# Kernel tuning notes

Measured on AMD Instinct MI355X. Metric: run time of the kernel, lower is better.

The kernel has to match this reference:

```python
import jax, jax.numpy as jnp
import numpy as np

V, E, H, L, B = 32000, 512, 512, 64, 32
H2 = 2 * H  # decoder hidden size
SOS = 127


def lstm_cell(x, h, c, Wih, Whh, b):
    gates = x @ Wih.T + h @ Whh.T + b
    i, f, g, o = jnp.split(gates, 4, axis=-1)
    i = jax.nn.sigmoid(i); f = jax.nn.sigmoid(f); o = jax.nn.sigmoid(o)
    g = jnp.tanh(g)
    c2 = f * c + i * g
    return o * jnp.tanh(c2), c2


def setup_inputs() -> dict:
    key = jax.random.key(0)
    ks = jax.random.split(key, 20)
    s = 0.02
    inp = {
        "x": jax.random.randint(ks[0], (B, L), 0, V),
        "enc_embed": s * jax.random.normal(ks[1], (V, E), jnp.float32),
        "ef_Wih": s * jax.random.normal(ks[2], (4 * H, E), jnp.float32),
        "ef_Whh": s * jax.random.normal(ks[3], (4 * H, H), jnp.float32),
        "ef_b": jnp.zeros((4 * H,), jnp.float32),
        "eb_Wih": s * jax.random.normal(ks[4], (4 * H, E), jnp.float32),
        "eb_Whh": s * jax.random.normal(ks[5], (4 * H, H), jnp.float32),
        "eb_b": jnp.zeros((4 * H,), jnp.float32),
        "dec_embed": s * jax.random.normal(ks[6], (V, H2), jnp.float32),
        "attn_W": s * jax.random.normal(ks[7], (L, 2 * H2), jnp.float32),
        "attn_b": jnp.zeros((L,), jnp.float32),
        "comb_W": s * jax.random.normal(ks[8], (H2, 2 * H2), jnp.float32),
        "comb_b": jnp.zeros((H2,), jnp.float32),
        "d_Wih": s * jax.random.normal(ks[9], (4 * H2, H2), jnp.float32),
        "d_Whh": s * jax.random.normal(ks[10], (4 * H2, H2), jnp.float32),
        "d_b": jnp.zeros((4 * H2,), jnp.float32),
        "out_W": s * jax.random.normal(ks[11], (V, H2), jnp.float32),
        "out_b": jnp.zeros((V,), jnp.float32),
    }
    return inp


def reference(x, enc_embed, ef_Wih, ef_Whh, ef_b, eb_Wih, eb_Whh, eb_b,
              dec_embed, attn_W, attn_b, comb_W, comb_b,
              d_Wih, d_Whh, d_b, out_W, out_b):
    b, seq = x.shape
    emb = enc_embed[x]  # (B, L, E)

    # Encoder: per-timestep bidirectional LSTM cells (each length-1 call),
    # state carried across the unrolled timestep loop.
    def enc_step(carry, xt):
        hf, cf, hb, cb = carry
        hf, cf = lstm_cell(xt, hf, cf, ef_Wih, ef_Whh, ef_b)
        hb, cb = lstm_cell(xt, hb, cb, eb_Wih, eb_Whh, eb_b)
        return (hf, cf, hb, cb), jnp.concatenate([hf, hb], axis=-1)

    z = jnp.zeros((b, ef_Whh.shape[1]), emb.dtype)
    _, enc_outs = jax.lax.scan(enc_step, (z, z, z, z), emb.transpose(1, 0, 2))
    enc_outs = enc_outs.transpose(1, 0, 2)  # (B, L, 2H)

    # Decoder: Bahdanau-style attention + LSTM cell, greedy argmax feedback.
    h2 = d_Whh.shape[1]

    def dec_step(carry, _):
        h, c, tok = carry
        e = dec_embed[tok]  # (B, 2H)
        aw = jax.nn.softmax(jnp.concatenate([e, h], -1) @ attn_W.T + attn_b, axis=-1)  # (B, L)
        ctx = jnp.einsum('bl,bld->bd', aw, enc_outs)  # (B, 2H)
        comb = jax.nn.relu(jnp.concatenate([e, ctx], -1) @ comb_W.T + comb_b)
        h, c = lstm_cell(comb, h, c, d_Wih, d_Whh, d_b)
        logits = jax.nn.log_softmax(h @ out_W.T + out_b, axis=-1)  # (B, V)
        tok = jnp.argmax(logits, axis=-1)
        return (h, c, tok), logits

    h0 = jnp.zeros((b, h2), emb.dtype)
    tok0 = jnp.full((b,), SOS, dtype=x.dtype)
    _, logits = jax.lax.scan(dec_step, (h0, h0, tok0), None, length=seq)
    return logits.transpose(1, 0, 2)  # (B, T, V)
```

## Files before the change

### kernel.cpp

```cpp
#include <hip/hip_runtime.h>
#include <hip/hip_bf16.h>
#include <string.h>

typedef __bf16 bf16;
typedef __attribute__((ext_vector_type(8))) __bf16 bf16x8;
typedef __attribute__((ext_vector_type(2))) __bf16 bf16x2;
typedef __attribute__((ext_vector_type(4))) float  f32x4;
typedef unsigned long long u64;
typedef unsigned char u8;

#define DEV __device__ __forceinline__

constexpr int V = 32000, E = 512, H = 512, L = 64, NB = 32, H2 = 1024, T = 64, SOS = 127;
constexpr int GE = 4 * H;
constexpr int NBLK = 256;

constexpr size_t OFF_GIN    = 0;
constexpr size_t SZ_GIN     = (size_t)2*T*NB*GE*4;
constexpr size_t OFF_ENCOUT = OFF_GIN + SZ_GIN;
constexpr size_t SZ_ENCOUT  = (size_t)NB*L*H2*2;
constexpr size_t OFF_ENCH   = OFF_ENCOUT + SZ_ENCOUT;
constexpr size_t SZ_ENCH    = (size_t)2*2*NB*H*2;
constexpr size_t OFF_DECH   = OFF_ENCH + SZ_ENCH;
constexpr size_t SZ_DECH    = (size_t)2*NB*H2*2;
constexpr size_t OFF_CAT2   = OFF_DECH + SZ_DECH;
constexpr size_t SZ_CAT2    = (size_t)NB*2*H2*2;
constexpr size_t OFF_COMB   = OFF_CAT2 + SZ_CAT2;
constexpr size_t SZ_COMB    = (size_t)NB*H2*2;
constexpr size_t OFF_HH     = OFF_COMB + SZ_COMB;
constexpr size_t SZ_HH      = (size_t)NB*4*H2*4;
constexpr size_t OFF_PMAX   = OFF_HH + SZ_HH;
constexpr size_t SZ_P       = (size_t)2*NBLK*NB*4;
constexpr size_t OFF_PSUM   = OFF_PMAX + SZ_P;
constexpr size_t OFF_PIDX   = OFF_PSUM + SZ_P;
constexpr size_t OFF_LOGZ   = OFF_PIDX + SZ_P;
constexpr size_t SZ_LOGZ    = (size_t)T*NB*4;
constexpr size_t OFF_WEFIH  = OFF_LOGZ + SZ_LOGZ;
constexpr size_t SZ_WENC    = (size_t)GE*E*2;
constexpr size_t OFF_WEFHH  = OFF_WEFIH + SZ_WENC;
constexpr size_t OFF_WEBIH  = OFF_WEFHH + SZ_WENC;
constexpr size_t OFF_WEBHH  = OFF_WEBIH + SZ_WENC;
constexpr size_t OFF_WCOMB  = OFF_WEBHH + SZ_WENC;
constexpr size_t SZ_WCOMB   = (size_t)H2*2*H2*2;
constexpr size_t OFF_WDIH   = OFF_WCOMB + SZ_WCOMB;
constexpr size_t SZ_WDEC    = (size_t)4*H2*H2*2;
constexpr size_t OFF_WDHH   = OFF_WDIH + SZ_WDEC;
constexpr size_t OFF_WOUT   = OFF_WDHH + SZ_WDEC;
constexpr size_t OFF_WOUT8  = OFF_WOUT;
constexpr size_t SZ_WOUT8   = (size_t)V*1024;
constexpr size_t OFF_WDHH8  = OFF_WOUT8 + SZ_WOUT8;
constexpr size_t SZ_WOUT    = (size_t)V*H2*2;
constexpr size_t OFF_WATTN  = OFF_WOUT + SZ_WOUT;
constexpr size_t SZ_WATTN   = (size_t)L*2*H2*2;
constexpr size_t OFF_EMB2   = OFF_WATTN + SZ_WATTN;
constexpr size_t SZ_EMB2    = (size_t)T*NB*E*2;
constexpr size_t OFF_BAR    = OFF_EMB2 + SZ_EMB2;
constexpr int TAG_PT = 0, TAG_C2 = 8192, TAG_CB = 9216, TAG_H = 11264, TAG_E = 13312;
constexpr int BAR_INTS = 15360;
constexpr size_t OFF_H8 = OFF_BAR + 131072;

constexpr int SM_CATF = 65536;
constexpr int SM_REDM = 73728;
constexpr int SM_REDS = 75776;
constexpr int SM_REDI = 77824;
constexpr int SM_SCR  = 79872;
constexpr int SM_HL   = 114688;
constexpr int SM_BYTES = 147456;

DEV f32x4 mfma16(bf16x8 a, bf16x8 b, f32x4 c) {
  return __builtin_amdgcn_mfma_f32_16x16x32_bf16(a, b, c, 0, 0, 0);
}
DEV f32x4 mfma8(long a, long b, f32x4 c) {
  return __builtin_amdgcn_mfma_f32_16x16x32_fp8_fp8(a, b, c, 0, 0, 0);
}
DEV float sigm(float x) { return 1.f / (1.f + __expf(-x)); }
DEV bf16x8 ld8(const bf16* p) { return *(const bf16x8*)p; }

union U16 { u64 u[2]; bf16x8 v8; f32x4 f4; };
union U4  { unsigned int u; bf16x2 v2; float f; };

DEV bf16x8 ld8_dev(const bf16* p) {
  U16 r;
  r.u[0] = __hip_atomic_load((const u64*)p,       __ATOMIC_RELAXED, __HIP_MEMORY_SCOPE_AGENT);
  r.u[1] = __hip_atomic_load((const u64*)(p + 4), __ATOMIC_RELAXED, __HIP_MEMORY_SCOPE_AGENT);
  return r.v8;
}
DEV void st8_dev(bf16* p, bf16x8 v) {
  U16 r; r.v8 = v;
  __hip_atomic_store((u64*)p,       r.u[0], __ATOMIC_RELAXED, __HIP_MEMORY_SCOPE_AGENT);
  __hip_atomic_store((u64*)(p + 4), r.u[1], __ATOMIC_RELAXED, __HIP_MEMORY_SCOPE_AGENT);
}
DEV void st16f_dev(float* p, f32x4 v) {
  U16 r; r.f4 = v;
  __hip_atomic_store((u64*)p,       r.u[0], __ATOMIC_RELAXED, __HIP_MEMORY_SCOPE_AGENT);
  __hip_atomic_store((u64*)(p + 2), r.u[1], __ATOMIC_RELAXED, __HIP_MEMORY_SCOPE_AGENT);
}
DEV float ldf_dev(const float* p) {
  return __hip_atomic_load(p, __ATOMIC_RELAXED, __HIP_MEMORY_SCOPE_AGENT);
}
DEV void stf_dev(float* p, float v) {
  __hip_atomic_store(p, v, __ATOMIC_RELAXED, __HIP_MEMORY_SCOPE_AGENT);
}
DEV int ldi_dev(const int* p) {
  return __hip_atomic_load(p, __ATOMIC_RELAXED, __HIP_MEMORY_SCOPE_AGENT);
}
DEV void sti_dev(int* p, int v) {
  __hip_atomic_store(p, v, __ATOMIC_RELAXED, __HIP_MEMORY_SCOPE_AGENT);
}
DEV void stb_dev(bf16* p, float x) {
  bf16 h = (bf16)x; unsigned short s; memcpy(&s, &h, 2);
  __hip_atomic_store((unsigned short*)p, s, __ATOMIC_RELAXED, __HIP_MEMORY_SCOPE_AGENT);
}
DEV void st2b_dev(bf16* p, bf16x2 v) {
  U4 r; r.v2 = v;
  __hip_atomic_store((unsigned int*)p, r.u, __ATOMIC_RELAXED, __HIP_MEMORY_SCOPE_AGENT);
}
DEV void stb8_dev(u8* p, u8 v) {
  __hip_atomic_store(p, v, __ATOMIC_RELAXED, __HIP_MEMORY_SCOPE_AGENT);
}
DEV u64 ldu64_dev(const u8* p) {
  return __hip_atomic_load((const u64*)p, __ATOMIC_RELAXED, __HIP_MEMORY_SCOPE_AGENT);
}

DEV void tpub(int* tags, int slot, int ep) {
  __syncthreads();
  if (threadIdx.x == 0)
    sti_dev(tags + slot*32, ep);
}
DEV void twait(int* tags, int n, int ep) {
  if ((int)threadIdx.x < n)
    while (ldi_dev(tags + threadIdx.x*32) < ep)
      __builtin_amdgcn_s_sleep(1);
  asm volatile("" ::: "memory");
  __syncthreads();
}

struct ConvJobs { const float* src[7]; bf16* dst[7]; long n8[7]; };

__global__ __launch_bounds__(256) void k_convert_all(ConvJobs J) {
  long i0 = (long)blockIdx.x * 256 + threadIdx.x;
  long stride = (long)gridDim.x * 256;
  for (int j = 0; j < 7; ++j) {
    const float* __restrict__ src = J.src[j];
    bf16* __restrict__ dst = J.dst[j];
    long n8 = J.n8[j];
    for (long g = i0; g < n8; g += stride) {
      long o = g * 8;
      float4 a = *(const float4*)(src + o);
      float4 b = *(const float4*)(src + o + 4);
      bf16x8 v;
      v[0]=(bf16)a.x; v[1]=(bf16)a.y; v[2]=(bf16)a.z; v[3]=(bf16)a.w;
      v[4]=(bf16)b.x; v[5]=(bf16)b.y; v[6]=(bf16)b.z; v[7]=(bf16)b.w;
      *(bf16x8*)(dst + o) = v;
    }
  }
}

__global__ __launch_bounds__(256) void k_conv_fp8(const float* __restrict__ wsrc,
                                                  const float* __restrict__ hsrc,
                                                  u8* __restrict__ wdst,
                                                  u8* __restrict__ hdst) {
  const long G1 = (long)V*64, G2 = (long)4096*64;
  for (long id = (long)blockIdx.x*256 + threadIdx.x; id < G1 + G2;
       id += (long)gridDim.x*256) {
    const float* s; u8* d; long n, g;
    if (id < G1) { n = id >> 6; g = id & 63; s = wsrc + n*1024 + g*16;
                   d = wdst + n*1024 + ((g ^ (n & 7)) << 4); }
    else { long j = id - G1; n = j >> 6; g = j & 63; s = hsrc + n*1024 + g*16;
           d = hdst + n*1024 + ((g ^ (n & 7)) << 4); }
    unsigned int wv[4];
#pragma unroll
    for (int q = 0; q < 4; ++q) {
      float4 f = *(const float4*)(s + q*4);
      int lo = __builtin_amdgcn_cvt_pk_fp8_f32(f.x*8.f, f.y*8.f, 0, false);
      int hi = __builtin_amdgcn_cvt_pk_fp8_f32(f.z*8.f, f.w*8.f, 0, false);
      wv[q] = (lo & 0xFFFF) | (hi << 16);
    }
    *(uint4*)d = make_uint4(wv[0], wv[1], wv[2], wv[3]);
  }
}

__global__ __launch_bounds__(256) void k_gather_emb(const int* __restrict__ x,
                                                    const float* __restrict__ embed,
                                                    bf16* __restrict__ emb2) {
  int gid = blockIdx.x * 256 + threadIdx.x;
  int m = gid >> 6, k8 = (gid & 63) * 8;
  int b = m & 31, t = m >> 5;
  int tok = x[b * L + t];
  const float* src = embed + (long)tok * E + k8;
  float4 a = *(const float4*)src;
  float4 c = *(const float4*)(src + 4);
  bf16x8 v;
  v[0]=(bf16)a.x; v[1]=(bf16)a.y; v[2]=(bf16)a.z; v[3]=(bf16)a.w;
  v[4]=(bf16)c.x; v[5]=(bf16)c.y; v[6]=(bf16)c.z; v[7]=(bf16)c.w;
  *(bf16x8*)(emb2 + (long)m * E + k8) = v;
}

__global__ __launch_bounds__(256) void k_init(bf16* ench, bf16* dech, float* hh,
                                              int* bar) {
  int i = blockIdx.x * 256 + threadIdx.x;
  hh[i] = 0.f;
  if (i < 2*NB*H)  ench[i] = (bf16)0.f;
  if (i < NB*H2)   dech[i] = (bf16)0.f;
  if (i < BAR_INTS) bar[i] = 0;
}

__global__ __launch_bounds__(256) void k_enc_ingemm(
    const bf16* __restrict__ emb2,
    const bf16* __restrict__ fWih, const float* __restrict__ fB,
    const bf16* __restrict__ bWih, const float* __restrict__ bB,
    float* __restrict__ gin)
{
  int wid  = blockIdx.x * 4 + (threadIdx.x >> 6);
  int lane = threadIdx.x & 63;
  int dir  = wid >> 11;
  int w2   = wid & 2047;
  int m0   = (w2 >> 5) * 32;
  int n0   = (w2 & 31) * 64;
  const bf16*  Wih  = dir ? bWih : fWih;
  const float* Bias = dir ? bB : fB;
  int col = lane & 15, kq = lane >> 4, r4 = kq * 4;

  const bf16* arow[4];
#pragma unroll
  for (int nt = 0; nt < 4; ++nt) arow[nt] = Wih + (long)(n0 + nt*16 + col)*E + kq*8;
  const bf16* brow[2];
#pragma unroll
  for (int mt = 0; mt < 2; ++mt) brow[mt] = emb2 + (long)(m0 + mt*16 + col)*E + kq*8;

  f32x4 acc[2][4] = {};
  for (int kk = 0; kk < E/32; ++kk) {
    bf16x8 a[4], bv[2];
#pragma unroll
    for (int nt = 0; nt < 4; ++nt) a[nt] = ld8(arow[nt] + kk*32);
#pragma unroll
    for (int mt = 0; mt < 2; ++mt) bv[mt] = ld8(brow[mt] + kk*32);
#pragma unroll
    for (int mt = 0; mt < 2; ++mt)
#pragma unroll
      for (int nt = 0; nt < 4; ++nt)
        acc[mt][nt] = mfma16(a[nt], bv[mt], acc[mt][nt]);
  }
#pragma unroll
  for (int mt = 0; mt < 2; ++mt) {
    int m = m0 + mt*16 + col;
    int b = m & 31, t = m >> 5;
    float* gp = gin + ((long)(dir*T + t)*NB + b)*GE;
#pragma unroll
    for (int nt = 0; nt < 4; ++nt) {
      int nb = n0 + nt*16 + r4;
      f32x4 v = acc[mt][nt];
      float4 o;
      o.x = v[0] + Bias[nb+0];
      o.y = v[1] + Bias[nb+1];
      o.z = v[2] + Bias[nb+2];
      o.w = v[3] + Bias[nb+3];
      *(float4*)(gp + nb) = o;
    }
  }
}

struct EncArgs {
  const bf16* fWhh; const bf16* bWhh; const float* gin;
  bf16* ench; bf16* encout; int* etag;
};

__global__ __launch_bounds__(256, 1) void k_encoder(EncArgs A) {
  __shared__ float lds[4][16][32];
  int tid = threadIdx.x, w = tid >> 6, lane = tid & 63;
  int dir = blockIdx.x >> 5, j0 = (blockIdx.x & 31) * 16;
  int col = lane & 15, kq = lane >> 4, r4 = kq*4;
  const bf16* Whh = dir ? A.bWhh : A.fWhh;
  const bf16* arow = Whh + (long)(w*H + j0 + col)*H + kq*8;
  int* myTags = A.etag + dir*32*32;
  float creg0 = 0.f, creg1 = 0.f;

  for (int t = 0; t < T; ++t) {
    if (t > 0) twait(myTags, 32, t);
    const bf16* hbase = A.ench + (t&1)*(2*NB*H) + dir*(NB*H);
    bf16*       hout  = A.ench + ((t&1)^1)*(2*NB*H) + dir*(NB*H);
    const bf16* b0 = hbase + col*H + kq*8;
    const bf16* b1 = hbase + (16+col)*H + kq*8;
    f32x4 a0 = {}, a1 = {};
    for (int kk = 0; kk < H/32; ++kk) {
      bf16x8 a = ld8(arow + kk*32);
      a0 = mfma16(a, ld8_dev(b0 + kk*32), a0);
      a1 = mfma16(a, ld8_dev(b1 + kk*32), a1);
    }
#pragma unroll
    for (int r = 0; r < 4; ++r) { lds[w][r4+r][col] = a0[r]; lds[w][r4+r][16+col] = a1[r]; }
    __syncthreads();
    const float* gp = A.gin + (long)(dir*T + t)*NB*GE;
    {
      int jj = tid >> 5, b = tid & 31, j = j0 + jj;
      const float* g4 = gp + (long)b*GE;
      float i_ = sigm(lds[0][jj][b] + g4[0*H + j]);
      float f_ = sigm(lds[1][jj][b] + g4[1*H + j]);
      float g_ = tanhf(lds[2][jj][b] + g4[2*H + j]);
      float o_ = sigm(lds[3][jj][b] + g4[3*H + j]);
      float c2 = f_*creg0 + i_*g_; creg0 = c2;
      float hv = o_*tanhf(c2);
      stb_dev(hout + b*H + j, hv);
      A.encout[((long)b*L + t)*H2 + dir*H + j] = (bf16)hv;
    }
    {
      int idx = tid + 256, jj = idx >> 5, b = idx & 31, j = j0 + jj;
      const float* g4 = gp + (long)b*GE;
      float i_ = sigm(lds[0][jj][b] + g4[0*H + j]);
      float f_ = sigm(lds[1][jj][b] + g4[1*H + j]);
      float g_ = tanhf(lds[2][jj][b] + g4[2*H + j]);
      float o_ = sigm(lds[3][jj][b] + g4[3*H + j]);
      float c2 = f_*creg1 + i_*g_; creg1 = c2;
      float hv = o_*tanhf(c2);
      stb_dev(hout + b*H + j, hv);
      A.encout[((long)b*L + t)*H2 + dir*H + j] = (bf16)hv;
    }
    tpub(myTags, blockIdx.x & 31, t + 1);
  }
}

struct DecArgs {
  const float* dec_embed; const bf16* wattn; const float* attn_b;
  const bf16* encout;
  const bf16* wcomb; const float* comb_b;
  const bf16* wdih; const float* db;
  const u8* wout8; const u8* wdhh8; const float* outb;
  bf16* dech; u8* hout8; float* hh; bf16* cat2; bf16* comb;
  float* pmax; float* psum; int* pidx; float* logz; float* out;
  int* tags;
};

__global__ __launch_bounds__(512, 1) void k_decoder(DecArgs A) {
  __shared__ __attribute__((aligned(16))) char smem[SM_BYTES];
  __shared__ float aw[64];
  __shared__ int   stok;
  float* catF = (float*)(smem + SM_CATF);
  float* redm = (float*)(smem + SM_REDM);
  float* reds = (float*)(smem + SM_REDS);
  int*   redi = (int*)  (smem + SM_REDI);
  float* scr  = (float*)(smem + SM_SCR);

  int* PT  = A.tags + TAG_PT;
  int* C2T = A.tags + TAG_C2;
  int* CBT = A.tags + TAG_CB;
  int* HT  = A.tags + TAG_H;

  int tid = threadIdx.x, bid = blockIdx.x;
  int w = tid >> 6, lane = tid & 63;
  int col = lane & 15, kq = lane >> 4, r4 = kq*4;
  float creg = 0.f;

  int ntot = (bid < 48) ? 8 : 9;
  int tstart = (bid < 48) ? bid*8 : 384 + 9*(bid - 48);
  int nlds = (bid < 64) ? 4 : 7;

  for (int i = 0; i < nlds; ++i) {
    int tn = tstart + i;
    const u8* src = (tn < 2000) ? A.wout8 + (long)tn*16384
                                : A.wdhh8 + (long)(tn - 2000)*16384;
#pragma unroll
    for (int rr = 0; rr < 2; ++rr) {
      int flat = rr*8192 + w*1024 + lane*16;
      __builtin_amdgcn_global_load_lds(
          (const __attribute__((address_space(1))) void*)(src + flat),
          (__attribute__((address_space(3))) void*)(smem + i*16384 + rr*8192 + w*1024),
          16, 0, 0);
    }
  }
  asm volatile("s_waitcnt vmcnt(0)" ::: "memory");
  __syncthreads();

  for (int t = 0; t < T; ++t) {
    const bf16* hin  = A.dech + (t&1)*(NB*H2);
    bf16*       hout = A.dech + ((t&1)^1)*(NB*H2);
    float* pmaxP = A.pmax + ((t&1)^1)*NBLK*32;
    float* psumP = A.psum + ((t&1)^1)*NBLK*32;
    int*   pidxP = A.pidx + ((t&1)^1)*NBLK*32;

    if (bid < NB) {
      int b = bid;
      if (t > 0) {
        twait(PT, NBLK, t);
        float m = -1e30f, s = 0.f; int id = 0;
        for (int c = tid; c < NBLK; c += 512) {
          float cm = ldf_dev(pmaxP + c*32 + b); int ci = ldi_dev(pidxP + c*32 + b);
          s += ldf_dev(psumP + c*32 + b);
          if (cm > m || (cm == m && ci < id)) { m = cm; id = ci; }
        }
        redm[tid] = m; reds[tid] = s; redi[tid] = id;
        __syncthreads();
        for (int off = 256; off; off >>= 1) {
          if (tid < off) {
            float om = redm[tid+off]; int oi = redi[tid+off];
            reds[tid] += reds[tid+off];
            if (om > redm[tid] || (om == redm[tid] && oi < redi[tid])) { redm[tid]=om; redi[tid]=oi; }
          }
          __syncthreads();
        }
        if (tid == 0) { A.logz[(t-1)*32 + b] = logf(reds[0]); stok = redi[0]; }
      } else if (tid == 0) stok = SOS;
      __syncthreads();
      int tok = stok;

      const float* erow = A.dec_embed + (long)tok*H2;
      bf16* c2row = A.cat2 + (long)b*(2*H2);
      if (tid < 128) {
        int o = tid*8;
        float4 a = *(const float4*)(erow + o);
        float4 c = *(const float4*)(erow + o + 4);
        catF[o+0]=a.x; catF[o+1]=a.y; catF[o+2]=a.z; catF[o+3]=a.w;
        catF[o+4]=c.x; catF[o+5]=c.y; catF[o+6]=c.z; catF[o+7]=c.w;
        bf16x8 v;
        v[0]=(bf16)a.x; v[1]=(bf16)a.y; v[2]=(bf16)a.z; v[3]=(bf16)a.w;
        v[4]=(bf16)c.x; v[5]=(bf16)c.y; v[6]=(bf16)c.z; v[7]=(bf16)c.w;
        st8_dev(c2row + o, v);
      } else if (tid < 256) {
        int o = (tid - 128)*8;
        bf16x8 hv = ld8_dev(hin + (long)b*H2 + o);
#pragma unroll
        for (int e = 0; e < 8; ++e) catF[H2 + o + e] = (float)hv[e];
      }
      __syncthreads();

      {
        int l = tid >> 3, q = tid & 7;
        const bf16*  wrow = A.wattn + (long)l*(2*H2) + q*256;
        const float* crow = catF + q*256;
        float sacc = 0.f;
        for (int k = 0; k < 256; k += 8) {
          bf16x8 wv = ld8(wrow + k);
#pragma unroll
          for (int e = 0; e < 8; ++e) sacc += (float)wv[e] * crow[k+e];
        }
        sacc += __shfl_xor(sacc, 1);
        sacc += __shfl_xor(sacc, 2);
        sacc += __shfl_xor(sacc, 4);
        if (q == 0) aw[l] = sacc + A.attn_b[l];
      }
      __syncthreads();

      if (tid < 64) {
        float v = aw[tid];
        float m = v;
#pragma unroll
        for (int off = 1; off < 64; off <<= 1) m = fmaxf(m, __shfl_xor(m, off));
        float p = __expf(v - m);
        float s = p;
#pragma unroll
        for (int off = 1; off < 64; off <<= 1) s += __shfl_xor(s, off);
        aw[tid] = p / s;
      }
      __syncthreads();

      {
        int grp = tid >> 7, jt = tid & 127;
        int j8 = jt * 8;
        const bf16* eo = A.encout + (long)b*L*H2 + j8;
        float acc[8] = {};
        for (int l = grp*16; l < grp*16 + 16; ++l) {
          float a = aw[l];
          bf16x8 v = ld8(eo + (long)l*H2);
#pragma unroll
          for (int e = 0; e < 8; ++e) acc[e] += a*(float)v[e];
        }
#pragma unroll
        for (int e = 0; e < 8; ++e) scr[grp*1024 + j8 + e] = acc[e];
      }
      __syncthreads();
      {
        int j2 = tid * 2;
        bf16x2 o;
#pragma unroll
        for (int e = 0; e < 2; ++e) {
          int j = j2 + e;
          o[e] = (bf16)(scr[j] + scr[1024+j] + scr[2048+j] + scr[3072+j]);
        }
        st2b_dev(c2row + H2 + j2, o);
      }
      tpub(C2T, bid, t + 1);
    }

    if (bid < 64) {
      twait(C2T, 32, t + 1);
      int n0 = bid * 16;
      const bf16* arow = A.wcomb + (long)(n0 + col)*(2*H2) + w*256 + kq*8;
      const bf16* b0 = A.cat2 + (long)col*(2*H2) + w*256 + kq*8;
      const bf16* b1 = A.cat2 + (long)(16+col)*(2*H2) + w*256 + kq*8;
      f32x4 a0 = {}, a1 = {};
      for (int kk = 0; kk < 8; ++kk) {
        bf16x8 a = ld8(arow + kk*32);
        a0 = mfma16(a, ld8_dev(b0 + kk*32), a0);
        a1 = mfma16(a, ld8_dev(b1 + kk*32), a1);
      }
#pragma unroll
      for (int r = 0; r < 4; ++r) {
        scr[(w*2+0)*256 + (r4+r)*16 + col] = a0[r];
        scr[(w*2+1)*256 + (r4+r)*16 + col] = a1[r];
      }
      __syncthreads();
      {
        int r = tid >> 5, b = tid & 31;
        int bt = b >> 4, cb = b & 15;
        float v = 0.f;
#pragma unroll
        for (int g = 0; g < 8; ++g) v += scr[(g*2+bt)*256 + r*16 + cb];
        v += A.comb_b[n0 + r];
        stb_dev(A.comb + (long)b*H2 + n0 + r, fmaxf(v, 0.f));
      }
      tpub(CBT, bid, t + 1);
    }

    if (bid < 64) {
      twait(CBT, 64, t + 1);
      int j0 = bid * 16;
      int g = w >> 1, half = w & 1;
      const bf16* arow = A.wdih + (long)(g*H2 + j0 + col)*H2 + half*512 + kq*8;
      const bf16* b0 = A.comb + (long)col*H2 + half*512 + kq*8;
      const bf16* b1 = A.comb + (long)(16+col)*H2 + half*512 + kq*8;
      f32x4 a0 = {}, a1 = {};
      for (int kk = 0; kk < 16; ++kk) {
        bf16x8 a = ld8(arow + kk*32);
        a0 = mfma16(a, ld8_dev(b0 + kk*32), a0);
        a1 = mfma16(a, ld8_dev(b1 + kk*32), a1);
      }
#pragma unroll
      for (int r = 0; r < 4; ++r) {
        scr[(w*2+0)*256 + (r4+r)*16 + col] = a0[r];
        scr[(w*2+1)*256 + (r4+r)*16 + col] = a1[r];
      }
      __syncthreads();
      {
        int jj = tid >> 5, b = tid & 31, j = j0 + jj;
        int bt = b >> 4, cb = b & 15;
#define GV(gg) (scr[((2*(gg)+0)*2+bt)*256 + jj*16 + cb] + scr[((2*(gg)+1)*2+bt)*256 + jj*16 + cb] \
                + A.db[(gg)*H2 + j] + ldf_dev(A.hh + (long)b*(4*H2) + (gg)*H2 + j))
        float i_ = sigm(GV(0));
        float f_ = sigm(GV(1));
        float g_ = tanhf(GV(2));
        float o_ = sigm(GV(3));
#undef GV
        float c2 = f_*creg + i_*g_; creg = c2;
        float hv = o_*tanhf(c2);
        stb_dev(hout + b*H2 + j, hv);
        int q8 = __builtin_amdgcn_cvt_pk_fp8_f32(hv*16.f, hv*16.f, 0, false);
        stb8_dev(A.hout8 + b*1024 + j, (u8)(q8 & 0xFF));
      }
      tpub(HT, bid, t + 1);
    }

    {
      twait(HT, 64, t + 1);
      float* pmaxW = A.pmax + (t&1)*NBLK*32;
      float* psumW = A.psum + (t&1)*NBLK*32;
      int*   pidxW = A.pidx + (t&1)*NBLK*32;

#pragma unroll
      for (int k2 = 0; k2 < 4; ++k2) {
        int id = k2*512 + tid;
        int r = id >> 6, g = id & 63;
        const u8* sp = A.hout8 + r*1024 + g*16;
        u64 lo = ldu64_dev(sp);
        u64 hi = ldu64_dev(sp + 8);
        char* dp = smem + SM_HL + r*1024 + ((g ^ (r & 7)) << 4);
        *(u64*)dp = lo; *(u64*)(dp + 8) = hi;
      }
      __syncthreads();

      float pm[2] = {-1e30f, -1e30f};
      float ps[2] = {0.f, 0.f};
      int  pid[2] = {0, 0};

      for (int ii = 0; ii < 2; ++ii) {
        if (ii == 1 && (w != 0 || ntot < 9)) break;
        int ti = (ii == 0) ? w : 8;
        int tn = tstart + ti;
        f32x4 acc0 = {}, acc1 = {};
        if (ti < nlds) {
          const char* Ab = smem + ti*16384 + col*1024;
          const char* Hb = smem + SM_HL + col*1024;
#pragma unroll 8
          for (int ks = 0; ks < 32; ++ks) {
            int off = (((ks*2 + (kq>>1)) ^ (col & 7)) << 4) + (kq & 1)*8;
            long a  = *(const long*)(Ab + off);
            long b0 = *(const long*)(Hb + off);
            long b1 = *(const long*)(Hb + 16*1024 + off);
            acc0 = mfma8(a, b0, acc0);
            acc1 = mfma8(a, b1, acc1);
          }
        } else {
          const u8* Ab = ((tn < 2000) ? A.wout8 + (long)tn*16384
                                      : A.wdhh8 + (long)(tn - 2000)*16384) + col*1024;
          const char* Hb = smem + SM_HL + col*1024;
#pragma unroll 8
          for (int ks = 0; ks < 32; ++ks) {
            int off = (((ks*2 + (kq>>1)) ^ (col & 7)) << 4) + (kq & 1)*8;
            long a  = *(const long*)(Ab + off);
            long b0 = *(const long*)(Hb + off);
            long b1 = *(const long*)(Hb + 16*1024 + off);
            acc0 = mfma8(a, b0, acc0);
            acc1 = mfma8(a, b1, acc1);
          }
        }
        if (tn < 2000) {
          int nb = tn*16 + kq*4;
#pragma unroll
          for (int bt = 0; bt < 2; ++bt) {
            int b = col + bt*16;
            f32x4 v = bt ? acc1 : acc0;
            f32x4 o;
#pragma unroll
            for (int r = 0; r < 4; ++r) {
              float xv = v[r]*0.0078125f + A.outb[nb + r];
              o[r] = xv;
              ps[bt] += __expf(xv);
              if (xv > pm[bt]) { pm[bt] = xv; pid[bt] = nb + r; }
            }
            __builtin_nontemporal_store(o, (f32x4*)(A.out + ((long)b*T + t)*V + nb));
          }
        } else {
          int nb = (tn - 2000)*16 + kq*4;
#pragma unroll
          for (int bt = 0; bt < 2; ++bt) {
            int b = col + bt*16;
            f32x4 v = bt ? acc1 : acc0;
#pragma unroll
            for (int r = 0; r < 4; ++r) v[r] *= 0.0078125f;
            st16f_dev(A.hh + (long)b*(4*H2) + nb, v);
          }
        }
      }
#pragma unroll
      for (int off = 16; off <= 32; off <<= 1) {
#pragma unroll
        for (int bt = 0; bt < 2; ++bt) {
          float om = __shfl_xor(pm[bt], off);
          float os = __shfl_xor(ps[bt], off);
          int   oi = __shfl_xor(pid[bt], off);
          ps[bt] += os;
          if (om > pm[bt] || (om == pm[bt] && oi < pid[bt])) { pm[bt] = om; pid[bt] = oi; }
        }
      }
      __syncthreads();
      float* dm = (float*)(smem + SM_HL);
      float* ds = dm + 256;
      int*   di = (int*)(ds + 256);
      if (lane < 16) {
#pragma unroll
        for (int bt = 0; bt < 2; ++bt) {
          int b = bt*16 + lane;
          dm[w*32 + b] = pm[bt];
          ds[w*32 + b] = ps[bt];
          di[w*32 + b] = pid[bt];
        }
      }
      __syncthreads();
      if (tid < 32) {
        int b = tid;
        float m = -1e30f, s = 0.f; int id = 0;
#pragma unroll
        for (int r = 0; r < 8; ++r) {
          float om = dm[r*32 + b]; int oi = di[r*32 + b];
          s += ds[r*32 + b];
          if (om > m || (om == m && oi < id)) { m = om; id = oi; }
        }
        stf_dev(pmaxW + bid*32 + b, m);
        stf_dev(psumW + bid*32 + b, s);
        sti_dev(pidxW + bid*32 + b, id);
      }
      tpub(PT, bid, t + 1);
    }
  }

  if (bid < NB) {
    twait(PT, NBLK, T);
    int b = bid;
    const float* psumP = A.psum + ((T-1)&1)*NBLK*32;
    float s = 0.f;
    for (int c = tid; c < NBLK; c += 512) s += ldf_dev(psumP + c*32 + b);
    reds[tid] = s;
    __syncthreads();
    for (int off = 256; off; off >>= 1) {
      if (tid < off) reds[tid] += reds[tid+off];
      __syncthreads();
    }
    if (tid == 0) A.logz[(T-1)*32 + b] = logf(reds[0]);
  }
}

__global__ __launch_bounds__(256) void k_fixup(float* __restrict__ out,
                                               const float* __restrict__ logz)
{
  long i = (long)blockIdx.x * 256 + threadIdx.x;
  long stride = (long)gridDim.x * 256;
  long total = (long)NB * T * V / 4;
  for (long g = i; g < total; g += stride) {
    long flat = g * 4;
    long bt = flat / V;
    int tt = (int)(bt & 63), b = (int)(bt >> 6);
    float lz = logz[tt*32 + b];
    f32x4 v = *(const f32x4*)(out + flat);
    v[0] -= lz; v[1] -= lz; v[2] -= lz; v[3] -= lz;
    __builtin_nontemporal_store(v, (f32x4*)(out + flat));
  }
}

extern "C" void kernel_launch(void* const* d_in, const int* in_sizes, int n_in,
                              void* d_out, int out_size, void* d_ws, size_t ws_size,
                              hipStream_t stream)
{
  const int*   x         = (const int*)  d_in[0];
  const float* enc_embed = (const float*)d_in[1];
  const float* ef_Wih    = (const float*)d_in[2];
  const float* ef_Whh    = (const float*)d_in[3];
  const float* ef_b      = (const float*)d_in[4];
  const float* eb_Wih    = (const float*)d_in[5];
  const float* eb_Whh    = (const float*)d_in[6];
  const float* eb_b      = (const float*)d_in[7];
  const float* dec_embed = (const float*)d_in[8];
  const float* attn_W    = (const float*)d_in[9];
  const float* attn_b    = (const float*)d_in[10];
  const float* comb_W    = (const float*)d_in[11];
  const float* comb_b    = (const float*)d_in[12];
  const float* d_Wih     = (const float*)d_in[13];
  const float* d_Whh     = (const float*)d_in[14];
  const float* d_b       = (const float*)d_in[15];
  const float* out_W     = (const float*)d_in[16];
  const float* out_b     = (const float*)d_in[17];
  float* out = (float*)d_out;
  char* ws = (char*)d_ws;

  float* gin    = (float*)(ws + OFF_GIN);
  bf16*  encout = (bf16*) (ws + OFF_ENCOUT);
  bf16*  ench   = (bf16*) (ws + OFF_ENCH);
  bf16*  dech   = (bf16*) (ws + OFF_DECH);
  bf16*  cat2   = (bf16*) (ws + OFF_CAT2);
  bf16*  comb   = (bf16*) (ws + OFF_COMB);
  float* hh     = (float*)(ws + OFF_HH);
  float* pmax   = (float*)(ws + OFF_PMAX);
  float* psum   = (float*)(ws + OFF_PSUM);
  int*   pidx   = (int*)  (ws + OFF_PIDX);
  float* logz   = (float*)(ws + OFF_LOGZ);
  bf16*  wefih  = (bf16*) (ws + OFF_WEFIH);
  bf16*  wefhh  = (bf16*) (ws + OFF_WEFHH);
  bf16*  webih  = (bf16*) (ws + OFF_WEBIH);
  bf16*  webhh  = (bf16*) (ws + OFF_WEBHH);
  bf16*  wcomb  = (bf16*) (ws + OFF_WCOMB);
  bf16*  wdih   = (bf16*) (ws + OFF_WDIH);
  u8*    wout8  = (u8*)   (ws + OFF_WOUT8);
  u8*    wdhh8  = (u8*)   (ws + OFF_WDHH8);
  bf16*  wattn  = (bf16*) (ws + OFF_WATTN);
  bf16*  emb2   = (bf16*) (ws + OFF_EMB2);
  int*   bar    = (int*)  (ws + OFF_BAR);
  u8*    hout8  = (u8*)   (ws + OFF_H8);

  ConvJobs J;
  J.src[0]=ef_Wih; J.dst[0]=wefih; J.n8[0]=(long)GE*E/8;
  J.src[1]=ef_Whh; J.dst[1]=wefhh; J.n8[1]=(long)GE*H/8;
  J.src[2]=eb_Wih; J.dst[2]=webih; J.n8[2]=(long)GE*E/8;
  J.src[3]=eb_Whh; J.dst[3]=webhh; J.n8[3]=(long)GE*H/8;
  J.src[4]=comb_W; J.dst[4]=wcomb; J.n8[4]=(long)H2*2*H2/8;
  J.src[5]=d_Wih;  J.dst[5]=wdih;  J.n8[5]=(long)4*H2*H2/8;
  J.src[6]=attn_W; J.dst[6]=wattn; J.n8[6]=(long)L*2*H2/8;
  hipLaunchKernelGGL(k_convert_all, dim3(2048), dim3(256), 0, stream, J);
  hipLaunchKernelGGL(k_conv_fp8, dim3(2048), dim3(256), 0, stream,
                     out_W, d_Whh, wout8, wdhh8);
  hipLaunchKernelGGL(k_gather_emb, dim3(512), dim3(256), 0, stream, x, enc_embed, emb2);
  hipLaunchKernelGGL(k_init, dim3(512), dim3(256), 0, stream, ench, dech, hh, bar);
  hipLaunchKernelGGL(k_enc_ingemm, dim3(1024), dim3(256), 0, stream,
                     emb2, wefih, ef_b, webih, eb_b, gin);

  EncArgs EA = { wefhh, webhh, gin, ench, encout, bar + TAG_E };
  hipLaunchKernelGGL(k_encoder, dim3(64), dim3(256), 0, stream, EA);

  DecArgs DA = { dec_embed, wattn, attn_b, encout, wcomb, comb_b,
                 wdih, d_b, wout8, wdhh8, out_b,
                 dech, hout8, hh, cat2, comb, pmax, psum, pidx, logz, out,
                 bar };
  hipLaunchKernelGGL(k_decoder, dim3(256), dim3(512), 0, stream, DA);

  hipLaunchKernelGGL(k_fixup, dim3(2048), dim3(256), 0, stream, out, logz);
}
```

Baseline: 5.212 ms.

## Cache all 7 weight tiles in LDS per block and use wave-shuffle reductions

Moves the scratch LDS regions (catF, reduction buffers, scratch) to overlap the SM_HL area so every block can keep 7 fp8 weight tiles resident in LDS, not 4 for the first 64 blocks. This removes per-timestep global weight streaming for those blocks. The argmax/logsumexp cross-block reduction now uses wave shuffles plus a 4-entry final pass instead of a 9-step shared-memory tree with a barrier at each step. The remaining global weight load uses a device-scope atomic load helper. Overlapping catF and the reduction buffers with SM_HL risks aliasing unless their lifetimes are disjoint.

```diff
diff --git a/kernel.cpp b/kernel.cpp
--- a/kernel.cpp
+++ b/kernel.cpp
@@ -59,12 +59,12 @@
 constexpr int BAR_INTS = 15360;
 constexpr size_t OFF_H8 = OFF_BAR + 131072;
 
-constexpr int SM_CATF = 65536;
-constexpr int SM_REDM = 73728;
-constexpr int SM_REDS = 75776;
-constexpr int SM_REDI = 77824;
-constexpr int SM_SCR  = 79872;
 constexpr int SM_HL   = 114688;
+constexpr int SM_CATF = 114688;
+constexpr int SM_REDM = 122880;
+constexpr int SM_REDS = 124928;
+constexpr int SM_REDI = 126976;
+constexpr int SM_SCR  = 129024;
 constexpr int SM_BYTES = 147456;
 
 DEV f32x4 mfma16(bf16x8 a, bf16x8 b, f32x4 c) {
@@ -352,7 +352,7 @@
 
   int ntot = (bid < 48) ? 8 : 9;
   int tstart = (bid < 48) ? bid*8 : 384 + 9*(bid - 48);
-  int nlds = (bid < 64) ? 4 : 7;
+  const int nlds = 7;
 
   for (int i = 0; i < nlds; ++i) {
     int tn = tstart + i;
@@ -382,22 +382,31 @@
       if (t > 0) {
         twait(PT, NBLK, t);
         float m = -1e30f, s = 0.f; int id = 0;
-        for (int c = tid; c < NBLK; c += 512) {
-          float cm = ldf_dev(pmaxP + c*32 + b); int ci = ldi_dev(pidxP + c*32 + b);
-          s += ldf_dev(psumP + c*32 + b);
-          if (cm > m || (cm == m && ci < id)) { m = cm; id = ci; }
-        }
-        redm[tid] = m; reds[tid] = s; redi[tid] = id;
+        if (tid < 256) {
+          m  = ldf_dev(pmaxP + tid*32 + b);
+          s  = ldf_dev(psumP + tid*32 + b);
+          id = ldi_dev(pidxP + tid*32 + b);
+#pragma unroll
+          for (int off = 1; off < 64; off <<= 1) {
+            float om = __shfl_xor(m, off);
+            float os = __shfl_xor(s, off);
+            int   oi = __shfl_xor(id, off);
+            s += os;
+            if (om > m || (om == m && oi < id)) { m = om; id = oi; }
+          }
+          if (lane == 0) { redm[w] = m; reds[w] = s; redi[w] = id; }
+        }
         __syncthreads();
-        for (int off = 256; off; off >>= 1) {
-          if (tid < off) {
-            float om = redm[tid+off]; int oi = redi[tid+off];
-            reds[tid] += reds[tid+off];
-            if (om > redm[tid] || (om == redm[tid] && oi < redi[tid])) { redm[tid]=om; redi[tid]=oi; }
+        if (tid == 0) {
+          float mm = redm[0]; int ii2 = redi[0];
+          float ss = reds[0] + reds[1] + reds[2] + reds[3];
+#pragma unroll
+          for (int q = 1; q < 4; ++q) {
+            if (redm[q] > mm || (redm[q] == mm && redi[q] < ii2)) { mm = redm[q]; ii2 = redi[q]; }
           }
-          __syncthreads();
-        }
-        if (tid == 0) { A.logz[(t-1)*32 + b] = logf(reds[0]); stok = redi[0]; }
+          A.logz[(t-1)*32 + b] = logf(ss);
+          stok = ii2;
+        }
       } else if (tid == 0) stok = SOS;
       __syncthreads();
       int tok = stok;
@@ -594,7 +603,7 @@
 #pragma unroll 8
           for (int ks = 0; ks < 32; ++ks) {
             int off = (((ks*2 + (kq>>1)) ^ (col & 7)) << 4) + (kq & 1)*8;
-            long a  = *(const long*)(Ab + off);
+            long a  = (long)ldu64_dev(Ab + off);
             long b0 = *(const long*)(Hb + off);
             long b1 = *(const long*)(Hb + 16*1024 + off);
             acc0 = mfma8(a, b0, acc0);
@@ -676,14 +685,14 @@
     int b = bid;
     const float* psumP = A.psum + ((T-1)&1)*NBLK*32;
     float s = 0.f;
-    for (int c = tid; c < NBLK; c += 512) s += ldf_dev(psumP + c*32 + b);
-    reds[tid] = s;
+    if (tid < 256) {
+      s = ldf_dev(psumP + tid*32 + b);
+#pragma unroll
+      for (int off = 1; off < 64; off <<= 1) s += __shfl_xor(s, off);
+      if (lane == 0) reds[w] = s;
+    }
     __syncthreads();
-    for (int off = 256; off; off >>= 1) {
-      if (tid < off) reds[tid] += reds[tid+off];
-      __syncthreads();
-    }
-    if (tid == 0) A.logz[(T-1)*32 + b] = logf(reds[0]);
+    if (tid == 0) A.logz[(T-1)*32 + b] = logf(reds[0] + reds[1] + reds[2] + reds[3]);
   }
 }
 
```

Result: faster. 4.812 ms, median of 2 (-7.7%).
